# Performance work log

Hardware: AMD Instinct MI355X
Metric: run time of the kernel (lower is better)

Reference implementation:

```python
import jax, jax.numpy as jnp
import numpy as np

D_MODEL = 1024
N_HEAD = 16
D_K = D_MODEL // N_HEAD
MAX_LEN = 1000
LN_EPS = 1e-5


def setup_inputs() -> dict:
    key = jax.random.key(0)
    ks = jax.random.split(key, 12)
    B, S = 4, 1000
    def xavier(k, shape):
        fan_in, fan_out = shape[1], shape[0]
        lim = np.sqrt(6.0 / (fan_in + fan_out))
        return jax.random.uniform(k, shape, jnp.float32, -lim, lim)
    return {
        "q": jax.random.normal(ks[0], (B, S, D_MODEL), jnp.float32),
        "k": jax.random.normal(ks[1], (B, S, D_MODEL), jnp.float32),
        "v": jax.random.normal(ks[2], (B, S, D_MODEL), jnp.float32),
        "ln_g": jnp.ones((D_MODEL,), jnp.float32),
        "ln_b": jnp.zeros((D_MODEL,), jnp.float32),
        "wq": xavier(ks[3], (D_MODEL, D_MODEL)),
        "bq": jnp.zeros((D_MODEL,), jnp.float32),
        "wk": xavier(ks[4], (D_MODEL, D_MODEL)),
        "bk": jnp.zeros((D_MODEL,), jnp.float32),
        "wv": xavier(ks[5], (D_MODEL, D_MODEL)),
        "bv": jnp.zeros((D_MODEL,), jnp.float32),
        "wo": xavier(ks[6], (D_MODEL, D_MODEL)),
        "bo": jnp.zeros((D_MODEL,), jnp.float32),
        "rel_emb": jax.random.normal(ks[7], (2 * MAX_LEN - 1, D_K), jnp.float32) / np.sqrt(D_K),
    }


def _layer_norm(x, g, b):
    mu = jnp.mean(x, axis=-1, keepdims=True)
    var = jnp.mean(jnp.square(x - mu), axis=-1, keepdims=True)
    return (x - mu) * jax.lax.rsqrt(var + LN_EPS) * g + b


def reference(q, k, v, ln_g, ln_b, wq, bq, wk, bk, wv, bv, wo, bo, rel_emb):
    B, S, _ = q.shape
    residual = q
    qn = _layer_norm(q, ln_g, ln_b)
    kn = _layer_norm(k, ln_g, ln_b)
    vn = _layer_norm(v, ln_g, ln_b)
    # torch Linear: y = x @ W^T + b; reshape to [B, H, S, d_k]
    def proj(x, w, b):
        return (x @ w.T + b).reshape(B, S, N_HEAD, D_K).transpose(0, 2, 1, 3)
    qh = proj(qn, wq, bq)
    kh = proj(kn, wk, bk)
    vh = proj(vn, wv, bv)
    scale = 1.0 / np.sqrt(D_K)
    scores = jnp.einsum('bhid,bhjd->bhij', qh, kh) * scale
    # relative position bias: rel_pos[i, j] = emb[center + (i - j)]
    center = MAX_LEN - 1
    start = center - (S - 1)
    window = jax.lax.dynamic_slice_in_dim(rel_emb, start, 2 * S - 1, axis=0)  # [2S-1, d_k]
    pos = jnp.arange(S)
    rel_idx = pos[:, None] - pos[None, :] + (S - 1)  # [S, S] in [0, 2S-2]
    rel_pos = window[rel_idx]  # [S, S, d_k]
    scores = scores + jnp.einsum('bhik,ijk->bhij', qh, rel_pos) * scale
    attn = jax.nn.softmax(scores, axis=-1)
    out = jnp.einsum('bhij,bhjd->bhid', attn, vh)
    out = out.transpose(0, 2, 1, 3).reshape(B, S, D_MODEL)
    out = out @ wo.T + bo
    return out + residual
```

## Files before the change

kernel.cpp:

```cpp
#include <hip/hip_runtime.h>
#include <hip/hip_bf16.h>

#define D_MODEL 1024
#define N_HEAD  16
#define D_K     64
#define MAX_LEN 1000
#define B_      4
#define S_      1000
#define S_PAD   1024
#define M_PAD   (B_ * S_PAD)
#define M_REAL  (B_ * S_)
#define LN_EPS  1e-5f
#define SCALE_L2E 0.1803368801111204f
#define REL_ROWS (2*MAX_LEN-1)

typedef __attribute__((ext_vector_type(8))) short short8;
typedef __attribute__((ext_vector_type(4))) float f32x4;

__device__ __forceinline__ unsigned short f2b(float f) {
    unsigned u = __builtin_bit_cast(unsigned, f);
    u = (u + 0x7FFFu + ((u >> 16) & 1u)) >> 16;
    return (unsigned short)u;
}

__device__ __forceinline__ unsigned short f2b_trunc(float f) {
    return (unsigned short)(__builtin_bit_cast(unsigned, f) >> 16);
}

__device__ __forceinline__ float b2f(unsigned short u) {
    return __builtin_bit_cast(float, (unsigned)u << 16);
}

__device__ __forceinline__ f32x4 mfma16(short8 a, short8 b, f32x4 c) {
    return __builtin_amdgcn_mfma_f32_16x16x32_bf16(a, b, c, 0, 0, 0);
}

__device__ __forceinline__ void gload_lds16(const void* g, void* l) {
    __builtin_amdgcn_global_load_lds(
        (const __attribute__((address_space(1))) unsigned int*)g,
        (__attribute__((address_space(3))) unsigned int*)l, 16, 0, 0);
}

__global__ void cvt_all(const float* __restrict__ s0, const float* __restrict__ s1,
                        const float* __restrict__ s2, const float* __restrict__ s3,
                        const float* __restrict__ s4,
                        unsigned short* __restrict__ d0, unsigned short* __restrict__ d1,
                        unsigned short* __restrict__ d2, unsigned short* __restrict__ d3,
                        unsigned short* __restrict__ d4) {
    int y = blockIdx.y;
    const float* in; unsigned short* out; int n4;
    switch (y) {
        case 0: in = s0; out = d0; n4 = 262144; break;
        case 1: in = s1; out = d1; n4 = 262144; break;
        case 2: in = s2; out = d2; n4 = 262144; break;
        case 3: in = s3; out = d3; n4 = 262144; break;
        default: in = s4; out = d4; n4 = REL_ROWS * D_K / 4; break;
    }
    int i = blockIdx.x * blockDim.x + threadIdx.x;
    if (i >= n4) return;
    float4 v = ((const float4*)in)[i];
    ushort4 o;
    o.x = f2b(v.x); o.y = f2b(v.y); o.z = f2b(v.z); o.w = f2b(v.w);
    ((ushort4*)out)[i] = o;
}

__global__ void ln_all(const float* __restrict__ xq, const float* __restrict__ xk,
                       const float* __restrict__ xv, const float* __restrict__ g,
                       const float* __restrict__ beta,
                       unsigned short* __restrict__ yq, unsigned short* __restrict__ yk,
                       unsigned short* __restrict__ yv) {
    int which = blockIdx.y;
    const float* x = which == 0 ? xq : which == 1 ? xk : xv;
    unsigned short* y = which == 0 ? yq : which == 1 ? yk : yv;

    int r = blockIdx.x;
    int b = r >> 10, i = r & 1023;
    unsigned short* yr = y + (size_t)r * D_MODEL;
    int tid = threadIdx.x;
    if (i >= S_) {
#pragma unroll
        for (int l = 0; l < 4; ++l) yr[tid + l * 256] = 0;
        return;
    }
    const float* xr = x + ((size_t)b * S_ + i) * D_MODEL;
    float v[4];
    float s = 0.f, sq = 0.f;
#pragma unroll
    for (int l = 0; l < 4; ++l) {
        v[l] = xr[tid + l * 256];
        s += v[l];
        sq += v[l] * v[l];
    }
#pragma unroll
    for (int o = 32; o > 0; o >>= 1) {
        s += __shfl_down(s, o, 64);
        sq += __shfl_down(sq, o, 64);
    }
    __shared__ float rs[4], rq[4];
    if ((tid & 63) == 0) { rs[tid >> 6] = s; rq[tid >> 6] = sq; }
    __syncthreads();
    if (tid == 0) {
        rs[0] = rs[0] + rs[1] + rs[2] + rs[3];
        rq[0] = rq[0] + rq[1] + rq[2] + rq[3];
    }
    __syncthreads();
    float mu = rs[0] * (1.0f / D_MODEL);
    float var = rq[0] * (1.0f / D_MODEL) - mu * mu;
    float rstd = rsqrtf(var + LN_EPS);
#pragma unroll
    for (int l = 0; l < 4; ++l) {
        int c = tid + l * 256;
        yr[c] = f2b((v[l] - mu) * rstd * g[c] + beta[c]);
    }
}

template<int MODE>
__device__ __forceinline__ void gemm_body(
        const unsigned short* __restrict__ X, const unsigned short* __restrict__ W,
        const float* __restrict__ bias, const float* __restrict__ resid,
        unsigned short* __restrict__ Yb, float* __restrict__ Yf,
        unsigned short* As, unsigned short* Bs, int row0, int col0) {
    int tid = threadIdx.x;
    int lane = tid & 63, w = tid >> 6;
    int wr = w >> 1, wc = w & 1;
    int fr = lane & 15, fk = (lane >> 4) * 8;

    f32x4 acc[4][4];
#pragma unroll
    for (int fm = 0; fm < 4; ++fm)
#pragma unroll
        for (int fn = 0; fn < 4; ++fn) acc[fm][fn] = (f32x4)0.f;

    int c0 = (w * 2 + 0) * 64 + lane;
    int c1 = (w * 2 + 1) * 64 + lane;
    const unsigned short* xs0 = X + (size_t)(row0 + (c0 >> 2)) * 1024 + (c0 & 3) * 8;
    const unsigned short* xs1 = X + (size_t)(row0 + (c1 >> 2)) * 1024 + (c1 & 3) * 8;
    const unsigned short* ws0 = W + (size_t)(col0 + (c0 >> 2)) * 1024 + (c0 & 3) * 8;
    const unsigned short* ws1 = W + (size_t)(col0 + (c1 >> 2)) * 1024 + (c1 & 3) * 8;
    int do0 = (w * 2 + 0) * 512;
    int do1 = (w * 2 + 1) * 512;

    auto stage = [&](int buf, int k0) {
        gload_lds16(xs0 + k0, As + buf * 4096 + do0);
        gload_lds16(xs1 + k0, As + buf * 4096 + do1);
        gload_lds16(ws0 + k0, Bs + buf * 4096 + do0);
        gload_lds16(ws1 + k0, Bs + buf * 4096 + do1);
    };

    stage(0, 0);

    for (int it = 0; it < 32; ++it) {
        __syncthreads();
        if (it < 31) stage((it & 1) ^ 1, (it + 1) * 32);

        const unsigned short* Ab = As + (it & 1) * 4096;
        const unsigned short* Bb = Bs + (it & 1) * 4096;
        short8 a[4], b[4];
#pragma unroll
        for (int fm = 0; fm < 4; ++fm)
            a[fm] = *(const short8*)(Ab + (wr * 64 + fm * 16 + fr) * 32 + fk);
#pragma unroll
        for (int fn = 0; fn < 4; ++fn)
            b[fn] = *(const short8*)(Bb + (wc * 64 + fn * 16 + fr) * 32 + fk);
#pragma unroll
        for (int fm = 0; fm < 4; ++fm)
#pragma unroll
            for (int fn = 0; fn < 4; ++fn)
                acc[fm][fn] = mfma16(a[fm], b[fn], acc[fm][fn]);
    }

#pragma unroll
    for (int fm = 0; fm < 4; ++fm) {
#pragma unroll
        for (int fn = 0; fn < 4; ++fn) {
            int cg = col0 + wc * 64 + fn * 16 + fr;
            float bv = bias[cg];
#pragma unroll
            for (int r = 0; r < 4; ++r) {
                int rg = row0 + wr * 64 + fm * 16 + (lane >> 4) * 4 + r;
                float val = acc[fm][fn][r] + bv;
                int b_ = rg >> 10, i = rg & 1023;
                if (MODE == 0) {
                    int h = cg >> 6, d = cg & 63;
                    Yb[(((size_t)(b_ * N_HEAD + h)) * S_PAD + i) * D_K + d] = f2b(val);
                } else if (MODE == 1) {
                    int h = cg >> 6, d = cg & 63;
                    Yb[(((size_t)(b_ * N_HEAD + h)) * D_K + d) * S_PAD + i] = f2b(val);
                } else {
                    if (i < S_) {
                        size_t orow = (size_t)b_ * S_ + i;
                        Yf[orow * 1024 + cg] = val + resid[orow * 1024 + cg];
                    }
                }
            }
        }
    }
}

__global__ __launch_bounds__(256) void gemm_qkv(
        const unsigned short* __restrict__ qn, const unsigned short* __restrict__ kn,
        const unsigned short* __restrict__ vn,
        const unsigned short* __restrict__ wqb, const unsigned short* __restrict__ wkb,
        const unsigned short* __restrict__ wvb,
        const float* __restrict__ bq, const float* __restrict__ bk,
        const float* __restrict__ bv,
        unsigned short* __restrict__ qh, unsigned short* __restrict__ kh,
        unsigned short* __restrict__ vt) {
    __shared__ __align__(16) unsigned short As[2][128 * 32];
    __shared__ __align__(16) unsigned short Bs[2][128 * 32];
    int fid = blockIdx.x + (blockIdx.y << 3) + (blockIdx.z << 8);
    int swz = (fid & 7) * 96 + (fid >> 3);
    int bz = swz >> 8;
    int rem = swz & 255;
    int row0 = (rem >> 3) * 128, col0 = (rem & 7) * 128;
    if (bz == 0)
        gemm_body<0>(qn, wqb, bq, nullptr, qh, nullptr, As[0], Bs[0], row0, col0);
    else if (bz == 1)
        gemm_body<0>(kn, wkb, bk, nullptr, kh, nullptr, As[0], Bs[0], row0, col0);
    else
        gemm_body<1>(vn, wvb, bv, nullptr, vt, nullptr, As[0], Bs[0], row0, col0);
}

__global__ __launch_bounds__(256) void gemm_out(
        const unsigned short* __restrict__ X, const unsigned short* __restrict__ W,
        const float* __restrict__ bias, const float* __restrict__ resid,
        float* __restrict__ Yf) {
    __shared__ __align__(16) unsigned short As[2][128 * 32];
    __shared__ __align__(16) unsigned short Bs[2][128 * 32];
    int fid = blockIdx.x + (blockIdx.y << 3);
    int swz = (fid & 7) * 32 + (fid >> 3);
    int row0 = (swz >> 3) * 128, col0 = (swz & 7) * 128;
    gemm_body<2>(X, W, bias, resid, nullptr, Yf, As[0], Bs[0], row0, col0);
}

#define QRW 84
#define PW  72
__device__ __forceinline__ void attn_slab(
        const unsigned short* __restrict__ Kc, const unsigned short* __restrict__ Vc,
        unsigned short* __restrict__ qp, const short8 (*rl)[2],
        short8 aq0, short8 aq1, f32x4* accO, float* mrun, float* lrun,
        bool mask_needed, int j0, int fr, int fk8, int rgrp, int rsw) {
    f32x4 accS[4];
#pragma unroll
    for (int fj = 0; fj < 4; ++fj) accS[fj] = (f32x4)0.f;
    __builtin_amdgcn_s_setprio(1);
#pragma unroll
    for (int fj = 0; fj < 4; ++fj) {
        int kb = (fj * 16 + fr) * 64 + fk8;
        accS[fj] = mfma16(aq0, *(const short8*)(Kc + (kb ^ rsw)), accS[fj]);
        accS[fj] = mfma16(aq1, *(const short8*)(Kc + ((kb + 32) ^ rsw)), accS[fj]);
    }
#pragma unroll
    for (int fu = 0; fu < 5; ++fu) {
        f32x4 qr = (f32x4)0.f;
        qr = mfma16(aq0, rl[fu][0], qr);
        qr = mfma16(aq1, rl[fu][1], qr);
#pragma unroll
        for (int r = 0; r < 4; ++r)
            qp[(rgrp + r) * QRW + fu * 16 + fr] = f2b_trunc(qr[r]);
    }
    __builtin_amdgcn_s_setprio(0);

    float sc[4][4];
#pragma unroll
    for (int fj = 0; fj < 4; ++fj) {
        int j_loc = fj * 16 + fr;
#pragma unroll
        for (int r = 0; r < 4; ++r) {
            int col = rgrp + r - j_loc + 63;
            sc[fj][r] = (accS[fj][r] + b2f(qp[(rgrp + r) * QRW + col])) * SCALE_L2E;
        }
    }
    if (mask_needed) {
#pragma unroll
        for (int fj = 0; fj < 4; ++fj) {
            int j_loc = fj * 16 + fr;
            if (j0 + j_loc >= S_) {
#pragma unroll
                for (int r = 0; r < 4; ++r) sc[fj][r] = -3e38f;
            }
        }
    }

    float pm[4];
#pragma unroll
    for (int r = 0; r < 4; ++r)
        pm[r] = fmaxf(fmaxf(sc[0][r], sc[1][r]), fmaxf(sc[2][r], sc[3][r]));
#pragma unroll
    for (int mask = 1; mask <= 8; mask <<= 1)
#pragma unroll
        for (int r = 0; r < 4; ++r)
            pm[r] = fmaxf(pm[r], __shfl_xor(pm[r], mask, 64));

    float dmax = fmaxf(fmaxf(pm[0] - mrun[0], pm[1] - mrun[1]),
                       fmaxf(pm[2] - mrun[2], pm[3] - mrun[3]));
    if (!__all(dmax <= 8.0f)) {
#pragma unroll
        for (int r = 0; r < 4; ++r) {
            float mn = fmaxf(mrun[r], pm[r]);
            float scl = __builtin_amdgcn_exp2f(mrun[r] - mn);
            mrun[r] = mn;
            lrun[r] *= scl;
#pragma unroll
            for (int fd = 0; fd < 4; ++fd) accO[fd][r] *= scl;
        }
    }

    float rsum[4];
#pragma unroll
    for (int r = 0; r < 4; ++r) rsum[r] = 0.f;
#pragma unroll
    for (int fj = 0; fj < 4; ++fj) {
#pragma unroll
        for (int r = 0; r < 4; ++r) {
            float p = __builtin_amdgcn_exp2f(sc[fj][r] - mrun[r]);
            rsum[r] += p;
            qp[(rgrp + r) * PW + fj * 16 + fr] = f2b_trunc(p);
        }
    }
#pragma unroll
    for (int mask = 1; mask <= 8; mask <<= 1)
#pragma unroll
        for (int r = 0; r < 4; ++r)
            rsum[r] += __shfl_xor(rsum[r], mask, 64);
#pragma unroll
    for (int r = 0; r < 4; ++r) lrun[r] += rsum[r];

    short8 ap0 = *(const short8*)(qp + fr * PW + fk8);
    short8 ap1 = *(const short8*)(qp + fr * PW + 32 + fk8);
    __builtin_amdgcn_s_setprio(1);
#pragma unroll
    for (int fd = 0; fd < 4; ++fd) {
        int vb = (fd * 16 + fr) * 64 + fk8;
        accO[fd] = mfma16(ap0, *(const short8*)(Vc + (vb ^ rsw)), accO[fd]);
        accO[fd] = mfma16(ap1, *(const short8*)(Vc + ((vb + 32) ^ rsw)), accO[fd]);
    }
    __builtin_amdgcn_s_setprio(0);
}

__global__ __launch_bounds__(256, 2) void attn_mfma(
        const unsigned short* __restrict__ qh, const unsigned short* __restrict__ kh,
        const unsigned short* __restrict__ vt, const unsigned short* __restrict__ relb,
        unsigned short* __restrict__ aout) {
    __shared__ __align__(16) unsigned short Ks[2][64 * 64];
    __shared__ __align__(16) unsigned short Vs[2][64 * 64];
    __shared__ __align__(16) unsigned short QP[4][16 * QRW];

    int tid = threadIdx.x, lane = tid & 63, w = tid >> 6;
    int bid = blockIdx.x;
    int swz = (bid & 7) * 64 + (bid >> 3);
    int bh = swz >> 3;
    int i0a = (((swz & 7) * 8) + 2 * w) * 16;
    int fr = lane & 15, fk8 = (lane >> 4) * 8, rgrp = (lane >> 4) * 4;
    int rsw = (fr & 7) << 3;

    const unsigned short* kbase = kh + (size_t)bh * S_PAD * D_K;
    const unsigned short* vtbase = vt + (size_t)bh * D_K * S_PAD;

    const unsigned short* qpa = qh + ((size_t)bh * S_PAD + i0a + fr) * D_K + fk8;
    short8 aqa0 = *(const short8*)(qpa);
    short8 aqa1 = *(const short8*)(qpa + 32);
    const unsigned short* qpb = qpa + 16 * D_K;
    short8 aqb0 = *(const short8*)(qpb);
    short8 aqb1 = *(const short8*)(qpb + 32);

    f32x4 accOa[4], accOb[4];
    float mruna[4], lruna[4], mrunb[4], lrunb[4];
#pragma unroll
    for (int fd = 0; fd < 4; ++fd) { accOa[fd] = (f32x4)0.f; accOb[fd] = (f32x4)0.f; }
#pragma unroll
    for (int r = 0; r < 4; ++r) {
        mruna[r] = -3e38f; lruna[r] = 0.f;
        mrunb[r] = -3e38f; lrunb[r] = 0.f;
    }

    unsigned short* qp = QP[w];
    int row_in = lane >> 3, slot = lane & 7;

    auto stage = [&](int buf, int it2) {
        int j0s = it2 * 64;
#pragma unroll
        for (int cc = 0; cc < 2; ++cc) {
            int c = w * 2 + cc;
            int r = c * 8 + row_in;
            gload_lds16(kbase + (size_t)(j0s + r) * 64 + (slot ^ row_in) * 8,
                        &Ks[buf][c * 512]);
        }
#pragma unroll
        for (int cc = 0; cc < 2; ++cc) {
            int c = w * 2 + cc;
            int d = c * 8 + row_in;
            gload_lds16(vtbase + (size_t)d * S_PAD + j0s + (slot ^ row_in) * 8,
                        &Vs[buf][c * 512]);
        }
    };

    stage(0, 0);
    __syncthreads();

    for (int it = 0; it < 16; ++it) {
        int cur = it & 1, j0 = it * 64;
        bool mask_needed = (j0 + 63 >= S_);

        short8 rl[6][2];
        int ub = i0a - j0 + (S_ - D_K);
#pragma unroll
        for (int fu = 0; fu < 6; ++fu) {
            int u = ub + fu * 16 + fr;
            u = u < 0 ? 0 : (u > REL_ROWS - 1 ? REL_ROWS - 1 : u);
            const unsigned short* rp = relb + (size_t)u * D_K + fk8;
            rl[fu][0] = *(const short8*)(rp);
            rl[fu][1] = *(const short8*)(rp + 32);
        }
        __builtin_amdgcn_sched_barrier(0);

        if (it < 15) stage(cur ^ 1, it + 1);

        attn_slab(Ks[cur], Vs[cur], qp, rl, aqa0, aqa1, accOa, mruna, lruna,
                  mask_needed, j0, fr, fk8, rgrp, rsw);
        attn_slab(Ks[cur], Vs[cur], qp, rl + 1, aqb0, aqb1, accOb, mrunb, lrunb,
                  mask_needed, j0, fr, fk8, rgrp, rsw);

        __syncthreads();
    }

    int b_ = bh >> 4, h = bh & 15;
#pragma unroll
    for (int r = 0; r < 4; ++r) {
        float inva = 1.0f / lruna[r];
        float invb = 1.0f / lrunb[r];
        int ma = b_ * S_PAD + i0a + rgrp + r;
        int mb = ma + 16;
#pragma unroll
        for (int fd = 0; fd < 4; ++fd) {
            int c = h * D_K + fd * 16 + fr;
            aout[(size_t)ma * D_MODEL + c] = f2b(accOa[fd][r] * inva);
            aout[(size_t)mb * D_MODEL + c] = f2b(accOb[fd][r] * invb);
        }
    }
}

extern "C" void kernel_launch(void* const* d_in, const int* in_sizes, int n_in,
                              void* d_out, int out_size, void* d_ws, size_t ws_size,
                              hipStream_t stream) {
    const float* q    = (const float*)d_in[0];
    const float* k    = (const float*)d_in[1];
    const float* v    = (const float*)d_in[2];
    const float* ln_g = (const float*)d_in[3];
    const float* ln_b = (const float*)d_in[4];
    const float* wq   = (const float*)d_in[5];
    const float* bq   = (const float*)d_in[6];
    const float* wk   = (const float*)d_in[7];
    const float* bk   = (const float*)d_in[8];
    const float* wv   = (const float*)d_in[9];
    const float* bv   = (const float*)d_in[10];
    const float* wo   = (const float*)d_in[11];
    const float* bo   = (const float*)d_in[12];
    const float* rel  = (const float*)d_in[13];
    float* out = (float*)d_out;

    const size_t TSZ = (size_t)M_PAD * D_MODEL;
    unsigned short* ws   = (unsigned short*)d_ws;
    unsigned short* qn   = ws;
    unsigned short* kn   = qn + TSZ;
    unsigned short* vn   = kn + TSZ;
    unsigned short* qh   = vn + TSZ;
    unsigned short* kh   = qh + TSZ;
    unsigned short* vt   = kh + TSZ;
    unsigned short* aout = vt + TSZ;
    unsigned short* wqb  = aout + TSZ;
    unsigned short* wkb  = wqb + 1024 * 1024;
    unsigned short* wvb  = wkb + 1024 * 1024;
    unsigned short* wob  = wvb + 1024 * 1024;
    unsigned short* relb = wob + 1024 * 1024;

    cvt_all<<<dim3(1024, 5), 256, 0, stream>>>(wq, wk, wv, wo, rel,
                                               wqb, wkb, wvb, wob, relb);

    ln_all<<<dim3(M_PAD, 3), 256, 0, stream>>>(q, k, v, ln_g, ln_b, qn, kn, vn);

    gemm_qkv<<<dim3(8, 32, 3), 256, 0, stream>>>(qn, kn, vn, wqb, wkb, wvb,
                                                 bq, bk, bv, qh, kh, vt);

    attn_mfma<<<512, 256, 0, stream>>>(qh, kh, vt, relb, aout);

    gemm_out<<<dim3(8, 32), 256, 0, stream>>>(aout, wob, bo, q, out);
}
```

Baseline: 181.5 us.

## Split attention over two key halves and merge partial softmax results

Splits each attention block's key range into two halves, launching twice as many blocks. Each block writes unnormalized partial outputs plus running max and sum. A new combine kernel rescales and merges the two partials into the final attention output. This raises parallelism from 512 blocks to 1024 on a 256-CU device. The cost is an extra kernel launch, extra traffic for the partial buffers (reusing the qn/kn/vn workspace), and bf16 rounding of the unnormalized partials.

```diff
diff --git a/kernel.cpp b/kernel.cpp
--- a/kernel.cpp
+++ b/kernel.cpp
@@ -13,6 +13,7 @@
 #define LN_EPS  1e-5f
 #define SCALE_L2E 0.1803368801111204f
 #define REL_ROWS (2*MAX_LEN-1)
+#define NROWS   65536
 
 typedef __attribute__((ext_vector_type(8))) short short8;
 typedef __attribute__((ext_vector_type(4))) float f32x4;
@@ -341,16 +342,19 @@
 __global__ __launch_bounds__(256, 2) void attn_mfma(
         const unsigned short* __restrict__ qh, const unsigned short* __restrict__ kh,
         const unsigned short* __restrict__ vt, const unsigned short* __restrict__ relb,
-        unsigned short* __restrict__ aout) {
+        unsigned short* __restrict__ pO0, unsigned short* __restrict__ pO1,
+        float2* __restrict__ pml) {
     __shared__ __align__(16) unsigned short Ks[2][64 * 64];
     __shared__ __align__(16) unsigned short Vs[2][64 * 64];
     __shared__ __align__(16) unsigned short QP[4][16 * QRW];
 
     int tid = threadIdx.x, lane = tid & 63, w = tid >> 6;
     int bid = blockIdx.x;
-    int swz = (bid & 7) * 64 + (bid >> 3);
-    int bh = swz >> 3;
-    int i0a = (((swz & 7) * 8) + 2 * w) * 16;
+    int swz = (bid & 7) * 128 + (bid >> 3);
+    int jhalf = swz & 1;
+    int g = swz >> 1;
+    int bh = g >> 3;
+    int i0a = (((g & 7) * 8) + 2 * w) * 16;
     int fr = lane & 15, fk8 = (lane >> 4) * 8, rgrp = (lane >> 4) * 4;
     int rsw = (fr & 7) << 3;
 
@@ -376,9 +380,10 @@
 
     unsigned short* qp = QP[w];
     int row_in = lane >> 3, slot = lane & 7;
+    int jbase = jhalf << 9;
 
     auto stage = [&](int buf, int it2) {
-        int j0s = it2 * 64;
+        int j0s = jbase + it2 * 64;
 #pragma unroll
         for (int cc = 0; cc < 2; ++cc) {
             int c = w * 2 + cc;
@@ -398,8 +403,8 @@
     stage(0, 0);
     __syncthreads();
 
-    for (int it = 0; it < 16; ++it) {
-        int cur = it & 1, j0 = it * 64;
+    for (int it = 0; it < 8; ++it) {
+        int cur = it & 1, j0 = jbase + it * 64;
         bool mask_needed = (j0 + 63 >= S_);
 
         short8 rl[6][2];
@@ -414,7 +419,7 @@
         }
         __builtin_amdgcn_sched_barrier(0);
 
-        if (it < 15) stage(cur ^ 1, it + 1);
+        if (it < 7) stage(cur ^ 1, it + 1);
 
         attn_slab(Ks[cur], Vs[cur], qp, rl, aqa0, aqa1, accOa, mruna, lruna,
                   mask_needed, j0, fr, fk8, rgrp, rsw);
@@ -424,20 +429,46 @@
         __syncthreads();
     }
 
+    unsigned short* pO = jhalf ? pO1 : pO0;
+    float2* pmlh = pml + (jhalf << 16);
+#pragma unroll
+    for (int r = 0; r < 4; ++r) {
+        int Ra = (bh << 10) + i0a + rgrp + r;
+        int Rb = Ra + 16;
+#pragma unroll
+        for (int fd = 0; fd < 4; ++fd) {
+            pO[((size_t)Ra << 6) + fd * 16 + fr] = f2b(accOa[fd][r]);
+            pO[((size_t)Rb << 6) + fd * 16 + fr] = f2b(accOb[fd][r]);
+        }
+        if (fr == 0) {
+            pmlh[Ra] = float2{mruna[r], lruna[r]};
+            pmlh[Rb] = float2{mrunb[r], lrunb[r]};
+        }
+    }
+}
+
+__global__ __launch_bounds__(256) void attn_combine(
+        const unsigned short* __restrict__ pO0, const unsigned short* __restrict__ pO1,
+        const float2* __restrict__ pml, unsigned short* __restrict__ aout) {
+    int tid = threadIdx.x;
+    int R = blockIdx.x * 16 + (tid >> 4);
+    int dg = (tid & 15) * 4;
+    float2 ml0 = pml[R];
+    float2 ml1 = pml[NROWS + R];
+    float m = fmaxf(ml0.x, ml1.x);
+    float w0 = __builtin_amdgcn_exp2f(ml0.x - m);
+    float w1 = __builtin_amdgcn_exp2f(ml1.x - m);
+    float invl = 1.0f / (ml0.y * w0 + ml1.y * w1);
+    ushort4 a4 = *(const ushort4*)(pO0 + ((size_t)R << 6) + dg);
+    ushort4 b4 = *(const ushort4*)(pO1 + ((size_t)R << 6) + dg);
+    int bh = R >> 10, i = R & 1023;
     int b_ = bh >> 4, h = bh & 15;
-#pragma unroll
-    for (int r = 0; r < 4; ++r) {
-        float inva = 1.0f / lruna[r];
-        float invb = 1.0f / lrunb[r];
-        int ma = b_ * S_PAD + i0a + rgrp + r;
-        int mb = ma + 16;
-#pragma unroll
-        for (int fd = 0; fd < 4; ++fd) {
-            int c = h * D_K + fd * 16 + fr;
-            aout[(size_t)ma * D_MODEL + c] = f2b(accOa[fd][r] * inva);
-            aout[(size_t)mb * D_MODEL + c] = f2b(accOb[fd][r] * invb);
-        }
-    }
+    ushort4 o;
+    o.x = f2b((b2f(a4.x) * w0 + b2f(b4.x) * w1) * invl);
+    o.y = f2b((b2f(a4.y) * w0 + b2f(b4.y) * w1) * invl);
+    o.z = f2b((b2f(a4.z) * w0 + b2f(b4.z) * w1) * invl);
+    o.w = f2b((b2f(a4.w) * w0 + b2f(b4.w) * w1) * invl);
+    *(ushort4*)(aout + ((size_t)((b_ << 10) + i)) * 1024 + h * 64 + dg) = o;
 }
 
 extern "C" void kernel_launch(void* const* d_in, const int* in_sizes, int n_in,
@@ -474,6 +505,10 @@
     unsigned short* wob  = wvb + 1024 * 1024;
     unsigned short* relb = wob + 1024 * 1024;
 
+    unsigned short* pO0 = qn;
+    unsigned short* pO1 = kn;
+    float2* pml = (float2*)vn;
+
     cvt_all<<<dim3(1024, 5), 256, 0, stream>>>(wq, wk, wv, wo, rel,
                                                wqb, wkb, wvb, wob, relb);
 
@@ -482,7 +517,9 @@
     gemm_qkv<<<dim3(8, 32, 3), 256, 0, stream>>>(qn, kn, vn, wqb, wkb, wvb,
                                                  bq, bk, bv, qh, kh, vt);
 
-    attn_mfma<<<512, 256, 0, stream>>>(qh, kh, vt, relb, aout);
+    attn_mfma<<<1024, 256, 0, stream>>>(qh, kh, vt, relb, pO0, pO1, pml);
+
+    attn_combine<<<4096, 256, 0, stream>>>(pO0, pO1, pml, aout);
 
     gemm_out<<<dim3(8, 32), 256, 0, stream>>>(aout, wob, bo, q, out);
 }
```

Measured after the change: 189.0 us. 4.1% more time.

## Merge prep kernels, transpose rel-bias scratch layout, use DPP row reductions

Applied to the files above, without the earlier changes.

Merges the weight-conversion and layernorm kernels into one launch to save a launch and a tail. In attention, the relative-position scratch tile is stored transposed so each lane writes its four values as one packed 8-byte store instead of four scalar stores. Row max and row sum reductions use DPP row-rotate instead of ds_swizzle/shfl_xor, cutting LDS-routed cross-lane traffic. The transposed layout changes bank access patterns on the gather reads, which could add conflicts.

```diff
diff --git a/kernel.cpp b/kernel.cpp
--- a/kernel.cpp
+++ b/kernel.cpp
@@ -41,42 +41,48 @@
         (__attribute__((address_space(3))) unsigned int*)l, 16, 0, 0);
 }
 
-__global__ void cvt_all(const float* __restrict__ s0, const float* __restrict__ s1,
-                        const float* __restrict__ s2, const float* __restrict__ s3,
-                        const float* __restrict__ s4,
-                        unsigned short* __restrict__ d0, unsigned short* __restrict__ d1,
-                        unsigned short* __restrict__ d2, unsigned short* __restrict__ d3,
-                        unsigned short* __restrict__ d4) {
-    int y = blockIdx.y;
-    const float* in; unsigned short* out; int n4;
-    switch (y) {
-        case 0: in = s0; out = d0; n4 = 262144; break;
-        case 1: in = s1; out = d1; n4 = 262144; break;
-        case 2: in = s2; out = d2; n4 = 262144; break;
-        case 3: in = s3; out = d3; n4 = 262144; break;
-        default: in = s4; out = d4; n4 = REL_ROWS * D_K / 4; break;
-    }
-    int i = blockIdx.x * blockDim.x + threadIdx.x;
-    if (i >= n4) return;
-    float4 v = ((const float4*)in)[i];
-    ushort4 o;
-    o.x = f2b(v.x); o.y = f2b(v.y); o.z = f2b(v.z); o.w = f2b(v.w);
-    ((ushort4*)out)[i] = o;
-}
-
-__global__ void ln_all(const float* __restrict__ xq, const float* __restrict__ xk,
-                       const float* __restrict__ xv, const float* __restrict__ g,
-                       const float* __restrict__ beta,
-                       unsigned short* __restrict__ yq, unsigned short* __restrict__ yk,
-                       unsigned short* __restrict__ yv) {
-    int which = blockIdx.y;
+#define DPPROR(x, S) __builtin_bit_cast(float, __builtin_amdgcn_update_dpp( \
+        0, __builtin_bit_cast(int, (x)), 0x120 | (S), 0xF, 0xF, false))
+
+__global__ void prep_all(const float* __restrict__ wq, const float* __restrict__ wk,
+                         const float* __restrict__ wv, const float* __restrict__ wo,
+                         const float* __restrict__ rel,
+                         unsigned short* __restrict__ wqb, unsigned short* __restrict__ wkb,
+                         unsigned short* __restrict__ wvb, unsigned short* __restrict__ wob,
+                         unsigned short* __restrict__ relb,
+                         const float* __restrict__ xq, const float* __restrict__ xk,
+                         const float* __restrict__ xv, const float* __restrict__ g,
+                         const float* __restrict__ beta,
+                         unsigned short* __restrict__ yq, unsigned short* __restrict__ yk,
+                         unsigned short* __restrict__ yv) {
+    __shared__ float rs[4], rq[4];
+    int bid = blockIdx.x;
+    int tid = threadIdx.x;
+    if (bid < 5120) {
+        int y = bid >> 10;
+        const float* in; unsigned short* out; int n4;
+        switch (y) {
+            case 0: in = wq; out = wqb; n4 = 262144; break;
+            case 1: in = wk; out = wkb; n4 = 262144; break;
+            case 2: in = wv; out = wvb; n4 = 262144; break;
+            case 3: in = wo; out = wob; n4 = 262144; break;
+            default: in = rel; out = relb; n4 = REL_ROWS * D_K / 4; break;
+        }
+        int i = (bid & 1023) * 256 + tid;
+        if (i >= n4) return;
+        float4 v = ((const float4*)in)[i];
+        ushort4 o;
+        o.x = f2b(v.x); o.y = f2b(v.y); o.z = f2b(v.z); o.w = f2b(v.w);
+        ((ushort4*)out)[i] = o;
+        return;
+    }
+    int r2 = bid - 5120;
+    int which = r2 >> 12;
+    int r = r2 & 4095;
     const float* x = which == 0 ? xq : which == 1 ? xk : xv;
     unsigned short* y = which == 0 ? yq : which == 1 ? yk : yv;
-
-    int r = blockIdx.x;
     int b = r >> 10, i = r & 1023;
     unsigned short* yr = y + (size_t)r * D_MODEL;
-    int tid = threadIdx.x;
     if (i >= S_) {
 #pragma unroll
         for (int l = 0; l < 4; ++l) yr[tid + l * 256] = 0;
@@ -96,7 +102,6 @@
         s += __shfl_down(s, o, 64);
         sq += __shfl_down(sq, o, 64);
     }
-    __shared__ float rs[4], rq[4];
     if ((tid & 63) == 0) { rs[tid >> 6] = s; rq[tid >> 6] = sq; }
     __syncthreads();
     if (tid == 0) {
@@ -233,7 +238,8 @@
     gemm_body<2>(X, W, bias, resid, nullptr, Yf, As[0], Bs[0], row0, col0);
 }
 
-#define QRW 84
+#define QRT 20
+#define QPW 1600
 #define PW  72
 __device__ __forceinline__ void attn_slab(
         const unsigned short* __restrict__ Kc, const unsigned short* __restrict__ Vc,
@@ -255,9 +261,9 @@
         f32x4 qr = (f32x4)0.f;
         qr = mfma16(aq0, rl[fu][0], qr);
         qr = mfma16(aq1, rl[fu][1], qr);
-#pragma unroll
-        for (int r = 0; r < 4; ++r)
-            qp[(rgrp + r) * QRW + fu * 16 + fr] = f2b_trunc(qr[r]);
+        unsigned lo = ((unsigned)f2b_trunc(qr[1]) << 16) | f2b_trunc(qr[0]);
+        unsigned hi = ((unsigned)f2b_trunc(qr[3]) << 16) | f2b_trunc(qr[2]);
+        *(uint2*)(qp + (fu * 16 + fr) * QRT + rgrp) = uint2{lo, hi};
     }
     __builtin_amdgcn_s_setprio(0);
 
@@ -268,7 +274,7 @@
 #pragma unroll
         for (int r = 0; r < 4; ++r) {
             int col = rgrp + r - j_loc + 63;
-            sc[fj][r] = (accS[fj][r] + b2f(qp[(rgrp + r) * QRW + col])) * SCALE_L2E;
+            sc[fj][r] = (accS[fj][r] + b2f(qp[col * QRT + rgrp + r])) * SCALE_L2E;
         }
     }
     if (mask_needed) {
@@ -284,13 +290,14 @@
 
     float pm[4];
 #pragma unroll
-    for (int r = 0; r < 4; ++r)
-        pm[r] = fmaxf(fmaxf(sc[0][r], sc[1][r]), fmaxf(sc[2][r], sc[3][r]));
-#pragma unroll
-    for (int mask = 1; mask <= 8; mask <<= 1)
-#pragma unroll
-        for (int r = 0; r < 4; ++r)
-            pm[r] = fmaxf(pm[r], __shfl_xor(pm[r], mask, 64));
+    for (int r = 0; r < 4; ++r) {
+        float m0 = fmaxf(fmaxf(sc[0][r], sc[1][r]), fmaxf(sc[2][r], sc[3][r]));
+        m0 = fmaxf(m0, DPPROR(m0, 1));
+        m0 = fmaxf(m0, DPPROR(m0, 2));
+        m0 = fmaxf(m0, DPPROR(m0, 4));
+        m0 = fmaxf(m0, DPPROR(m0, 8));
+        pm[r] = m0;
+    }
 
     float dmax = fmaxf(fmaxf(pm[0] - mrun[0], pm[1] - mrun[1]),
                        fmaxf(pm[2] - mrun[2], pm[3] - mrun[3]));
@@ -319,12 +326,14 @@
         }
     }
 #pragma unroll
-    for (int mask = 1; mask <= 8; mask <<= 1)
-#pragma unroll
-        for (int r = 0; r < 4; ++r)
-            rsum[r] += __shfl_xor(rsum[r], mask, 64);
-#pragma unroll
-    for (int r = 0; r < 4; ++r) lrun[r] += rsum[r];
+    for (int r = 0; r < 4; ++r) {
+        float s0 = rsum[r];
+        s0 += DPPROR(s0, 1);
+        s0 += DPPROR(s0, 2);
+        s0 += DPPROR(s0, 4);
+        s0 += DPPROR(s0, 8);
+        lrun[r] += s0;
+    }
 
     short8 ap0 = *(const short8*)(qp + fr * PW + fk8);
     short8 ap1 = *(const short8*)(qp + fr * PW + 32 + fk8);
@@ -344,7 +353,7 @@
         unsigned short* __restrict__ aout) {
     __shared__ __align__(16) unsigned short Ks[2][64 * 64];
     __shared__ __align__(16) unsigned short Vs[2][64 * 64];
-    __shared__ __align__(16) unsigned short QP[4][16 * QRW];
+    __shared__ __align__(16) unsigned short QP[4][QPW];
 
     int tid = threadIdx.x, lane = tid & 63, w = tid >> 6;
     int bid = blockIdx.x;
@@ -474,10 +483,9 @@
     unsigned short* wob  = wvb + 1024 * 1024;
     unsigned short* relb = wob + 1024 * 1024;
 
-    cvt_all<<<dim3(1024, 5), 256, 0, stream>>>(wq, wk, wv, wo, rel,
-                                               wqb, wkb, wvb, wob, relb);
-
-    ln_all<<<dim3(M_PAD, 3), 256, 0, stream>>>(q, k, v, ln_g, ln_b, qn, kn, vn);
+    prep_all<<<5120 + 3 * 4096, 256, 0, stream>>>(
+        wq, wk, wv, wo, rel, wqb, wkb, wvb, wob, relb,
+        q, k, v, ln_g, ln_b, qn, kn, vn);
 
     gemm_qkv<<<dim3(8, 32, 3), 256, 0, stream>>>(qn, kn, vn, wqb, wkb, wvb,
                                                  bq, bk, bv, qh, kh, vt);
```

Result: faster. 165.5 us (-8.8%).
